# Kernel tuning notes

Hardware: AMD Instinct MI355X
Metric: run time of the kernel (lower is better)

## Reference

```python
import jax, jax.numpy as jnp
import numpy as np

B, T, D = 8, 16, 1024
N, K, H = 16, 8, 128   # q heads, kv heads, head dim
S = 8192               # cache size
CUR = 4096             # tokens already in cache
ROPE_THETA = 1000000
EPS = 1e-6
LARGE_NEGATIVE = jnp.finfo(jnp.bfloat16).min


def setup_inputs() -> dict:
    key = jax.random.key(0)
    ks = jax.random.split(key, 8)
    w = 0.02  # realistic weight scale
    return {
        "x": jax.random.normal(ks[0], (B, T, D), jnp.float32),
        "Wq": jax.random.normal(ks[1], (D, N, H), jnp.float32) * w,
        "Wk": jax.random.normal(ks[2], (D, K, H), jnp.float32) * w,
        "Wv": jax.random.normal(ks[3], (D, K, H), jnp.float32) * w,
        "Wo": jax.random.normal(ks[4], (N, H, D), jnp.float32) * w,
        "q_scale": jnp.ones((H,), jnp.float32),
        "k_scale": jnp.ones((H,), jnp.float32),
        "k_cache": jax.random.normal(ks[5], (B, S, K, H), jnp.float32),
        "v_cache": jax.random.normal(ks[6], (B, S, K, H), jnp.float32),
        "segment_ids": jnp.ones((B, T), jnp.int32),
        "start_ind": jnp.zeros((B,), jnp.int32),  # already resolved (= left_pads)
        "cur_ind": CUR,
    }


def _rmsnorm(x, scale, eps=EPS):
    xf = x.astype(jnp.float32)
    y = xf * jax.lax.rsqrt(jnp.mean(xf * xf, axis=-1, keepdims=True) + eps)
    return (y * scale).astype(x.dtype)


def _rope_sincos(positions, head_dim):
    frac = jnp.arange(0, head_dim, 2, dtype=jnp.float32) / head_dim
    inv_freq = 1.0 / (ROPE_THETA ** frac)
    ang = jnp.einsum("BT,k->BTk", positions.astype(jnp.float32), inv_freq,
                     precision=jax.lax.Precision.HIGHEST)
    return jnp.sin(ang), jnp.cos(ang)


def _apply_rope(x, sin, cos):
    x1, x2 = x[..., : x.shape[-1] // 2], x[..., x.shape[-1] // 2 :]
    sin, cos = sin[:, :, None, :], cos[:, :, None, :]
    return jnp.concatenate([x1 * cos - x2 * sin, x2 * cos + x1 * sin], axis=-1).astype(x.dtype)


def reference(x, Wq, Wk, Wv, Wo, q_scale, k_scale, k_cache, v_cache,
              segment_ids, start_ind, cur_ind):
    b, t, _ = x.shape
    n_rep = N // K
    scale = H ** -0.5

    # projections + per-head RMSNorm on q/k
    q = _rmsnorm(jnp.einsum("BTD,DNH->BTNH", x, Wq), q_scale)
    k = _rmsnorm(jnp.einsum("BSD,DKH->BSKH", x, Wk), k_scale)
    v = jnp.einsum("BSD,DKH->BSKH", x, Wv)

    # start index: resolved from left pads on first call
    left_pads = jnp.sum(jnp.cumsum(segment_ids != 0, axis=-1) == 0, -1).astype(jnp.int32)
    start = jnp.where(start_ind < 0, left_pads, start_ind)

    # positions from segment ids, offset by cache cursor
    rel = jax.vmap(lambda row: jnp.where(row != 0, jnp.arange(t) - jnp.argmax(row), 2 ** 30))(segment_ids)
    pos = rel + cur_ind
    sin, cos = _rope_sincos(pos, H)
    q = _apply_rope(q, sin, cos)
    k = _apply_rope(k, sin, cos)

    # KV cache append
    kc = jax.lax.dynamic_update_slice(k_cache, k, (0, cur_ind, 0, 0))
    vc = jax.lax.dynamic_update_slice(v_cache, v, (0, cur_ind, 0, 0))

    # GQA attention against full cache
    qg = q.reshape((b, t, K, n_rep, H))
    logits = jnp.einsum("BTKGH,BSKH->BTSKG", qg, kc) * scale

    q_pos = cur_ind + jnp.arange(t, dtype=jnp.int32)[None, :] - start[:, None]
    ts = jnp.arange(S, dtype=jnp.int32)
    kv_seg = (ts[None, :] >= start[:, None]) & (ts[None, :] < cur_ind + t)
    k_pos = ts[None, :] - start[:, None]
    causal = k_pos[:, None, :] <= q_pos[:, :, None]
    seg_mask = kv_seg[:, None, :] == segment_ids[:, :, None]
    mask = (causal & seg_mask)[:, :, :, None, None]

    logits = jnp.where(mask, logits, LARGE_NEGATIVE)
    w = jax.nn.softmax(logits.astype(jnp.float32), axis=2).astype(logits.dtype)
    o = jnp.einsum("BTSKG,BSKH->BTKGH", w, vc).reshape((b, t, N, H))
    return jnp.einsum("BTNH,NHD->BTD", o, Wo)
```

## Files before the change

kernel.cpp:

```cpp
#include <hip/hip_runtime.h>

#define BB 8
#define TT 16
#define DD 1024
#define NN 16
#define KHN 8
#define HH 128
#define SS 8192
#define NPART 16

typedef __attribute__((ext_vector_type(8))) short bf16x8;
typedef __attribute__((ext_vector_type(4))) float f32x4;

__device__ __forceinline__ unsigned short f2bf(float f) {
  unsigned u = __builtin_bit_cast(unsigned, f);
  u += 0x7FFFu + ((u >> 16) & 1u);
  return (unsigned short)(u >> 16);
}
__device__ __forceinline__ float bf2f(unsigned short h) {
  unsigned u = ((unsigned)h) << 16;
  return __builtin_bit_cast(float, u);
}
__device__ __forceinline__ f32x4 mfma16(bf16x8 a, bf16x8 b, f32x4 c) {
  return __builtin_amdgcn_mfma_f32_16x16x32_bf16(a, b, c, 0, 0, 0);
}
__device__ __forceinline__ unsigned cvt_pair(float a, float b) {
  unsigned r;
  asm("v_cvt_pk_bf16_f32 %0, %1, %2" : "=v"(r) : "v"(a), "v"(b));
  return r;
}
__device__ __forceinline__ void pack4(unsigned short* dst, float a, float b, float c, float d) {
  *(uint2*)dst = make_uint2(cvt_pair(a, b), cvt_pair(c, d));
}
__device__ __forceinline__ bf16x8 cvt8(const float4& lo, const float4& hi) {
  return __builtin_bit_cast(bf16x8,
      make_uint4(cvt_pair(lo.x, lo.y), cvt_pair(lo.z, lo.w),
                 cvt_pair(hi.x, hi.y), cvt_pair(hi.z, hi.w)));
}

__global__ __launch_bounds__(256) void k_wtrans(
    const float* __restrict__ Wq, const float* __restrict__ Wk,
    const float* __restrict__ Wv, const float* __restrict__ Wo,
    unsigned short* __restrict__ Wt1, unsigned short* __restrict__ Wt2) {
  __shared__ __align__(16) unsigned short Tl[64][66];
  const int tid = threadIdx.x;
  const int z = blockIdx.z;
  const float* src; int K, N; unsigned short* dst;
  if (z == 0)      { src = Wq; K = 1024; N = 2048; dst = Wt1; }
  else if (z == 1) { src = Wk; K = 1024; N = 1024; dst = Wt1 + (size_t)2048 * 1024; }
  else if (z == 2) { src = Wv; K = 1024; N = 1024; dst = Wt1 + (size_t)3072 * 1024; }
  else             { src = Wo; K = 2048; N = 1024; dst = Wt2; }
  const int n0 = blockIdx.x * 64, k0 = blockIdx.y * 64;
  if (n0 >= N || k0 >= K) return;
  {
    const int r = tid >> 4, c4 = (tid & 15) << 2;
#pragma unroll
    for (int p = 0; p < 4; ++p) {
      const int k = p * 16 + r;
      float4 f = *(const float4*)(src + (size_t)(k0 + k) * N + n0 + c4);
      pack4(&Tl[k][c4], f.x, f.y, f.z, f.w);
    }
  }
  __syncthreads();
  {
    const int c8 = tid & 7, nb = tid >> 3;
#pragma unroll
    for (int p = 0; p < 2; ++p) {
      const int n = p * 32 + nb;
      unsigned short tmp[8];
#pragma unroll
      for (int j = 0; j < 8; ++j) tmp[j] = Tl[c8 * 8 + j][n];
      unsigned short* dp = dst + (size_t)(n0 + n) * K + k0 + c8 * 8;
      *(uint4*)dp = *(const uint4*)&tmp[0];
    }
  }
}

__global__ __launch_bounds__(256) void k_qkv_gemm(
    const float* __restrict__ x, const unsigned short* __restrict__ Wt1,
    float* __restrict__ qkv) {
  const int tid = threadIdx.x, lane = tid & 63, wv = tid >> 6;
  const int cc = lane & 15, g = lane >> 4;
  const int m0 = blockIdx.x * 32, n0 = blockIdx.y * 128;
  const int rt = wv >> 1, cb0 = (wv & 1) * 64;
  const int m = m0 + rt * 16 + cc;
  f32x4 acc[4];
#pragma unroll
  for (int i = 0; i < 4; ++i) acc[i] = (f32x4)0.0f;

#pragma unroll 4
  for (int k0 = 0; k0 < 1024; k0 += 32) {
    float4 fa = *(const float4*)(x + (size_t)m * 1024 + k0 + g * 8);
    float4 fb = *(const float4*)(x + (size_t)m * 1024 + k0 + g * 8 + 4);
    bf16x8 af = cvt8(fa, fb);
#pragma unroll
    for (int ct = 0; ct < 4; ++ct) {
      const int n = n0 + cb0 + ct * 16 + cc;
      bf16x8 bf = *(const bf16x8*)(Wt1 + (size_t)n * 1024 + k0 + g * 8);
      acc[ct] = mfma16(af, bf, acc[ct]);
    }
  }
#pragma unroll
  for (int ct = 0; ct < 4; ++ct)
#pragma unroll
    for (int r = 0; r < 4; ++r) {
      int row = m0 + rt * 16 + g * 4 + r;
      int col = n0 + cb0 + ct * 16 + cc;
      qkv[(size_t)row * 4096 + col] = acc[ct][r];
    }
}

__global__ __launch_bounds__(128) void k_normrope(
    const float* __restrict__ qkv, const float* __restrict__ qs,
    const float* __restrict__ ks, const int* __restrict__ seg,
    const int* __restrict__ cur_p,
    unsigned short* __restrict__ qa, unsigned short* __restrict__ ka,
    unsigned short* __restrict__ va) {
  __shared__ float lv[128];
  __shared__ float red[2];
  const int row = blockIdx.x, b = row >> 4, t = row & 15;
  const int hid = blockIdx.y;
  const int h = threadIdx.x;
  float val;
  if (hid < 16)      val = qkv[row * 4096 + hid * 128 + h];
  else if (hid < 24) val = qkv[row * 4096 + 2048 + (hid - 16) * 128 + h];
  else               val = qkv[row * 4096 + 3072 + (hid - 24) * 128 + h];

  if (hid >= 24) {
    int kh = hid - 24;
    va[((b * KHN + kh) * TT + t) * 128 + h] = f2bf(val);
    return;
  }
  float ss = val * val;
#pragma unroll
  for (int m = 1; m < 64; m <<= 1) ss += __shfl_xor(ss, m, 64);
  int wid = threadIdx.x >> 6, lane = threadIdx.x & 63;
  if (lane == 0) red[wid] = ss;
  __syncthreads();
  float mean = (red[0] + red[1]) * (1.0f / 128.0f);
  float scl = (hid < 16) ? qs[h] : ks[h];
  float nrm = val * (1.0f / sqrtf(mean + 1e-6f)) * scl;
  lv[h] = nrm;
  __syncthreads();
  float prt = lv[h ^ 64];
  const int cur = cur_p[0];
  int first = TT;
#pragma unroll
  for (int i = TT - 1; i >= 0; --i)
    if (seg[b * TT + i] != 0) first = i;
  float posf;
  if (seg[b * TT + t] != 0) posf = (float)(t - first + cur);
  else                      posf = (float)(1073741824 + cur);
  int j = h & 63;
  float inv = powf(1.0e6f, -((float)j) * (1.0f / 64.0f));
  float ang = posf * inv;
  float sn = sinf(ang), cs = cosf(ang);
  float outv = (h < 64) ? (nrm * cs - prt * sn) : (nrm * cs + prt * sn);
  if (hid < 16) {
    int kh = hid >> 1, gq = hid & 1;
    qa[((b * KHN + kh) * 32 + gq * 16 + t) * 128 + h] =
        f2bf(outv * 0.08838834764831845f);
  } else {
    int kh = hid - 16;
    ka[((b * KHN + kh) * TT + t) * 128 + h] = f2bf(outv);
  }
}

__global__ __launch_bounds__(256, 2) void k_attn(
    const float* __restrict__ kcache, const float* __restrict__ vcache,
    const unsigned short* __restrict__ qa, const unsigned short* __restrict__ ka,
    const unsigned short* __restrict__ va, const int* __restrict__ seg,
    const int* __restrict__ sind, const int* __restrict__ cur_p,
    float* __restrict__ partO, float* __restrict__ partML) {
  __shared__ __align__(16) unsigned short Kl[4][32][132];
  __shared__ float mls[2][32][2];
  const int tid = threadIdx.x, wv = tid >> 6, lane = tid & 63;
  const int cc = lane & 15, g = lane >> 4;
  const int pair = blockIdx.x, b = pair >> 3, kh = pair & 7;
  const int qi = blockIdx.y;
  const int cur = cur_p[0];
  const int len = cur + TT;
  int start_b = sind[b];
  if (start_b < 0) {
    int first = TT;
#pragma unroll
    for (int i = TT - 1; i >= 0; --i)
      if (seg[b * TT + i] != 0) first = i;
    start_b = first;
  }
  const int NTt = (len + 31) >> 5;
  const int L = (NTt + NPART - 1) / NPART;
  const int tlo = qi * L;
  const int thi = (tlo + L < NTt) ? (tlo + L) : NTt;

  bf16x8 qf[2][4];
  {
    const unsigned short* qb = qa + ((size_t)pair * 32) * 128;
#pragma unroll
    for (int rb = 0; rb < 2; ++rb)
#pragma unroll
      for (int kk = 0; kk < 4; ++kk)
        qf[rb][kk] = *(const bf16x8*)(qb + (rb * 16 + cc) * 128 + kk * 32 + g * 8);
  }
  const float* kcb = kcache + (size_t)b * (SS * 1024) + kh * 128;
  const float* vcb = vcache + (size_t)b * (SS * 1024) + kh * 128;
  const unsigned short* knb = ka + (size_t)(b * KHN + kh) * (TT * 128);
  const unsigned short* vnb = va + (size_t)(b * KHN + kh) * (TT * 128);

  f32x4 acc[2][8];
  float mreg[2][4], lreg[2][4];
#pragma unroll
  for (int rb = 0; rb < 2; ++rb) {
#pragma unroll
    for (int hb = 0; hb < 8; ++hb) acc[rb][hb] = (f32x4)0.0f;
#pragma unroll
    for (int r = 0; r < 4; ++r) { mreg[rb][r] = -1e30f; lreg[rb][r] = 0.0f; }
  }

  for (int tile = tlo + wv; tile < thi; tile += 4) {
    const int ts0 = tile << 5;
    __builtin_amdgcn_wave_barrier();
    if (ts0 + 32 <= cur) {
#pragma unroll
      for (int i = 0; i < 16; ++i) {
        int ch = lane + (i << 6);
        int r = ch >> 5, c4 = (ch & 31) << 2;
        float4 f = *(const float4*)(kcb + (size_t)(ts0 + r) * 1024 + c4);
        pack4(&Kl[wv][r][c4], f.x, f.y, f.z, f.w);
      }
    } else {
#pragma unroll
      for (int i = 0; i < 16; ++i) {
        int ch = lane + (i << 6);
        int r = ch >> 5, c4 = (ch & 31) << 2;
        int ts = ts0 + r;
        if (ts < cur) {
          float4 f = *(const float4*)(kcb + (size_t)ts * 1024 + c4);
          pack4(&Kl[wv][r][c4], f.x, f.y, f.z, f.w);
        } else {
          int tr = ts - cur; if (tr > TT - 1) tr = TT - 1;
          ushort4 u = *(const ushort4*)(knb + tr * 128 + c4);
          *(ushort4*)&Kl[wv][r][c4] = u;
        }
      }
    }
    __builtin_amdgcn_wave_barrier();
    f32x4 s[2][2];
#pragma unroll
    for (int rb = 0; rb < 2; ++rb)
#pragma unroll
      for (int cb = 0; cb < 2; ++cb) s[rb][cb] = (f32x4)0.0f;
#pragma unroll
    for (int kk = 0; kk < 4; ++kk) {
#pragma unroll
      for (int cb = 0; cb < 2; ++cb) {
        const unsigned short* kp = &Kl[wv][cb * 16 + cc][kk * 32 + g * 8];
        uint2 lo = *(const uint2*)kp;
        uint2 hi = *(const uint2*)(kp + 4);
        bf16x8 kf = __builtin_bit_cast(bf16x8, make_uint4(lo.x, lo.y, hi.x, hi.y));
        s[0][cb] = mfma16(qf[0][kk], kf, s[0][cb]);
        s[1][cb] = mfma16(qf[1][kk], kf, s[1][cb]);
      }
    }
    bf16x8 vf[8];
    if (ts0 + 32 <= cur) {
#pragma unroll
      for (int hb = 0; hb < 8; ++hb) {
        const int hc = hb * 16 + cc;
        float v0 = vcb[(size_t)(ts0 + g * 8 + 0) * 1024 + hc];
        float v1 = vcb[(size_t)(ts0 + g * 8 + 1) * 1024 + hc];
        float v2 = vcb[(size_t)(ts0 + g * 8 + 2) * 1024 + hc];
        float v3 = vcb[(size_t)(ts0 + g * 8 + 3) * 1024 + hc];
        float v4 = vcb[(size_t)(ts0 + g * 8 + 4) * 1024 + hc];
        float v5 = vcb[(size_t)(ts0 + g * 8 + 5) * 1024 + hc];
        float v6 = vcb[(size_t)(ts0 + g * 8 + 6) * 1024 + hc];
        float v7 = vcb[(size_t)(ts0 + g * 8 + 7) * 1024 + hc];
        vf[hb] = __builtin_bit_cast(bf16x8,
            make_uint4(cvt_pair(v0, v1), cvt_pair(v2, v3),
                       cvt_pair(v4, v5), cvt_pair(v6, v7)));
      }
    } else {
#pragma unroll
      for (int hb = 0; hb < 8; ++hb) {
        const int hc = hb * 16 + cc;
        float vv[8];
#pragma unroll
        for (int j = 0; j < 8; ++j) {
          const int ts = ts0 + g * 8 + j;
          if (ts < cur) vv[j] = vcb[(size_t)ts * 1024 + hc];
          else { int tr = ts - cur; if (tr > TT - 1) tr = TT - 1; vv[j] = bf2f(vnb[tr * 128 + hc]); }
        }
        vf[hb] = __builtin_bit_cast(bf16x8,
            make_uint4(cvt_pair(vv[0], vv[1]), cvt_pair(vv[2], vv[3]),
                       cvt_pair(vv[4], vv[5]), cvt_pair(vv[6], vv[7])));
      }
    }
    float al[2][4];
#pragma unroll
    for (int rb = 0; rb < 2; ++rb) {
#pragma unroll
      for (int r = 0; r < 4; ++r) {
        const int tq = g * 4 + r;
#pragma unroll
        for (int cb = 0; cb < 2; ++cb) {
          int ts = ts0 + cb * 16 + cc;
          bool ok = (ts >= start_b) && (ts <= cur + tq);
          if (!ok) s[rb][cb][r] = -1e30f;
        }
        float tm = fmaxf(s[rb][0][r], s[rb][1][r]);
#pragma unroll
        for (int m = 1; m < 16; m <<= 1) tm = fmaxf(tm, __shfl_xor(tm, m, 64));
        float mn = fmaxf(mreg[rb][r], tm);
        float a = __expf(mreg[rb][r] - mn);
        float p0 = (s[rb][0][r] < -1e29f) ? 0.0f : __expf(s[rb][0][r] - mn);
        float p1 = (s[rb][1][r] < -1e29f) ? 0.0f : __expf(s[rb][1][r] - mn);
        s[rb][0][r] = p0; s[rb][1][r] = p1;
        float rs = p0 + p1;
#pragma unroll
        for (int m = 1; m < 16; m <<= 1) rs += __shfl_xor(rs, m, 64);
        lreg[rb][r] = lreg[rb][r] * a + rs;
        mreg[rb][r] = mn;
        al[rb][r] = a;
      }
    }
    __builtin_amdgcn_wave_barrier();
#pragma unroll
    for (int rb = 0; rb < 2; ++rb)
#pragma unroll
      for (int cb = 0; cb < 2; ++cb)
#pragma unroll
        for (int r = 0; r < 4; ++r)
          Kl[wv][rb * 16 + g * 4 + r][cb * 16 + cc] = f2bf(s[rb][cb][r]);
    __builtin_amdgcn_wave_barrier();
    bf16x8 pf[2];
#pragma unroll
    for (int rb = 0; rb < 2; ++rb) {
      const unsigned short* pp = &Kl[wv][rb * 16 + cc][g * 8];
      uint2 lo = *(const uint2*)pp;
      uint2 hi = *(const uint2*)(pp + 4);
      pf[rb] = __builtin_bit_cast(bf16x8, make_uint4(lo.x, lo.y, hi.x, hi.y));
    }
#pragma unroll
    for (int rb = 0; rb < 2; ++rb)
#pragma unroll
      for (int hb = 0; hb < 8; ++hb) {
        f32x4 t = acc[rb][hb];
#pragma unroll
        for (int r = 0; r < 4; ++r) t[r] *= al[rb][r];
        acc[rb][hb] = mfma16(pf[rb], vf[hb], t);
      }
  }

  float* Oscr = (float*)&Kl[0][0][0];
  auto dump = [&](int sid) {
#pragma unroll
    for (int rb = 0; rb < 2; ++rb)
#pragma unroll
      for (int hb = 0; hb < 8; ++hb)
#pragma unroll
        for (int r = 0; r < 4; ++r)
          Oscr[(sid * 32 + rb * 16 + g * 4 + r) * 128 + hb * 16 + cc] = acc[rb][hb][r];
    if (cc == 0) {
#pragma unroll
      for (int rb = 0; rb < 2; ++rb)
#pragma unroll
        for (int r = 0; r < 4; ++r) {
          mls[sid][rb * 16 + g * 4 + r][0] = mreg[rb][r];
          mls[sid][rb * 16 + g * 4 + r][1] = lreg[rb][r];
        }
    }
  };
  auto mergefrom = [&](int sid) {
    float a0s[2][4], a1s[2][4];
#pragma unroll
    for (int rb = 0; rb < 2; ++rb)
#pragma unroll
      for (int r = 0; r < 4; ++r) {
        int row = rb * 16 + g * 4 + r;
        float mp = mls[sid][row][0], lp = mls[sid][row][1];
        float M = fmaxf(mreg[rb][r], mp);
        float a0 = __expf(mreg[rb][r] - M), a1 = __expf(mp - M);
        lreg[rb][r] = lreg[rb][r] * a0 + lp * a1;
        mreg[rb][r] = M;
        a0s[rb][r] = a0; a1s[rb][r] = a1;
      }
#pragma unroll
    for (int rb = 0; rb < 2; ++rb)
#pragma unroll
      for (int hb = 0; hb < 8; ++hb)
#pragma unroll
        for (int r = 0; r < 4; ++r) {
          int row = rb * 16 + g * 4 + r;
          acc[rb][hb][r] = acc[rb][hb][r] * a0s[rb][r] +
                           Oscr[(sid * 32 + row) * 128 + hb * 16 + cc] * a1s[rb][r];
        }
  };
  __syncthreads();
  if (wv >= 2) dump(wv - 2);
  __syncthreads();
  if (wv < 2) mergefrom(wv);
  __syncthreads();
  if (wv == 1) dump(0);
  __syncthreads();
  if (wv == 0) {
    mergefrom(0);
    size_t pidx = (size_t)pair * NPART + qi;
#pragma unroll
    for (int rb = 0; rb < 2; ++rb)
#pragma unroll
      for (int hb = 0; hb < 8; ++hb)
#pragma unroll
        for (int r = 0; r < 4; ++r)
          partO[(pidx * 32 + rb * 16 + g * 4 + r) * 128 + hb * 16 + cc] = acc[rb][hb][r];
    if (cc == 0) {
#pragma unroll
      for (int rb = 0; rb < 2; ++rb)
#pragma unroll
        for (int r = 0; r < 4; ++r) {
          partML[pidx * 64 + (rb * 16 + g * 4 + r) * 2 + 0] = mreg[rb][r];
          partML[pidx * 64 + (rb * 16 + g * 4 + r) * 2 + 1] = lreg[rb][r];
        }
    }
  }
}

__global__ __launch_bounds__(256) void k_combine(
    const float* __restrict__ partO, const float* __restrict__ partML,
    unsigned short* __restrict__ obf) {
  __shared__ float sc[NPART][32];
  const int pair = blockIdx.x, b = pair >> 3, kh = pair & 7;
  const int isub = blockIdx.y;
  const int tid = threadIdx.x;
  if (tid < 32) {
    float mm[NPART], ll[NPART];
    float M = -3.0e38f;
#pragma unroll
    for (int p = 0; p < NPART; ++p) {
      mm[p] = partML[((size_t)pair * NPART + p) * 64 + tid * 2 + 0];
      ll[p] = partML[((size_t)pair * NPART + p) * 64 + tid * 2 + 1];
      M = fmaxf(M, mm[p]);
    }
    float denom = 0.0f;
#pragma unroll
    for (int p = 0; p < NPART; ++p) denom += __expf(mm[p] - M) * ll[p];
    float inv = (denom > 0.0f) ? 1.0f / denom : 0.0f;
#pragma unroll
    for (int p = 0; p < NPART; ++p) sc[p][tid] = __expf(mm[p] - M) * inv;
  }
  __syncthreads();
#pragma unroll
  for (int i = 0; i < 4; ++i) {
    int idx = tid + ((isub * 4 + i) << 8);
    int row = idx >> 7, hc = idx & 127;
    float o = 0.0f;
#pragma unroll
    for (int p = 0; p < NPART; ++p)
      o += partO[(((size_t)pair * NPART + p) * 32 + row) * 128 + hc] * sc[p][row];
    int gq = row >> 4, t = row & 15, n = kh * 2 + gq;
    obf[((b * TT + t) * NN + n) * 128 + hc] = f2bf(o);
  }
}

__global__ __launch_bounds__(256) void k_out_gemm(
    const unsigned short* __restrict__ obf, const unsigned short* __restrict__ Wt2,
    float* __restrict__ out) {
  const int tid = threadIdx.x, lane = tid & 63, wv = tid >> 6;
  const int cc = lane & 15, g = lane >> 4;
  const int m0 = blockIdx.x * 32, n0 = blockIdx.y * 64;
  const int rt = wv >> 1, cb0 = (wv & 1) * 32;
  const int m = m0 + rt * 16 + cc;
  f32x4 acc[2];
#pragma unroll
  for (int i = 0; i < 2; ++i) acc[i] = (f32x4)0.0f;

#pragma unroll 4
  for (int k0 = 0; k0 < 2048; k0 += 32) {
    bf16x8 af = *(const bf16x8*)(obf + (size_t)m * 2048 + k0 + g * 8);
#pragma unroll
    for (int ct = 0; ct < 2; ++ct) {
      const int d = n0 + cb0 + ct * 16 + cc;
      bf16x8 bf = *(const bf16x8*)(Wt2 + (size_t)d * 2048 + k0 + g * 8);
      acc[ct] = mfma16(af, bf, acc[ct]);
    }
  }
#pragma unroll
  for (int ct = 0; ct < 2; ++ct)
#pragma unroll
    for (int r = 0; r < 4; ++r)
      out[(size_t)(m0 + rt * 16 + g * 4 + r) * 1024 + n0 + cb0 + ct * 16 + cc] = acc[ct][r];
}

extern "C" void kernel_launch(void* const* d_in, const int* in_sizes, int n_in,
                              void* d_out, int out_size, void* d_ws, size_t ws_size,
                              hipStream_t stream) {
  (void)in_sizes; (void)n_in; (void)out_size; (void)ws_size;
  const float* x   = (const float*)d_in[0];
  const float* Wq  = (const float*)d_in[1];
  const float* Wk  = (const float*)d_in[2];
  const float* Wv  = (const float*)d_in[3];
  const float* Wo  = (const float*)d_in[4];
  const float* qs  = (const float*)d_in[5];
  const float* ks  = (const float*)d_in[6];
  const float* kc  = (const float*)d_in[7];
  const float* vc  = (const float*)d_in[8];
  const int* seg   = (const int*)d_in[9];
  const int* sind  = (const int*)d_in[10];
  const int* curp  = (const int*)d_in[11];
  float* out = (float*)d_out;

  char* ws = (char*)d_ws;
  float*          qkv    = (float*)(ws + 0);
  unsigned short* qa     = (unsigned short*)(ws + 2097152);
  unsigned short* ka     = (unsigned short*)(ws + 2621440);
  unsigned short* va     = (unsigned short*)(ws + 2883584);
  float*          partO  = (float*)(ws + 3145728);
  float*          partML = (float*)(ws + 19922944);
  unsigned short* obf    = (unsigned short*)(ws + 20185088);
  unsigned short* Wt1    = (unsigned short*)(ws + 20709376);
  unsigned short* Wt2    = (unsigned short*)(ws + 29097984);

  k_wtrans<<<dim3(32, 32, 4), 256, 0, stream>>>(Wq, Wk, Wv, Wo, Wt1, Wt2);
  k_qkv_gemm<<<dim3(4, 32), 256, 0, stream>>>(x, Wt1, qkv);
  k_normrope<<<dim3(128, 32), 128, 0, stream>>>(qkv, qs, ks, seg, curp, qa, ka, va);
  k_attn<<<dim3(64, NPART), 256, 0, stream>>>(kc, vc, qa, ka, va, seg, sind, curp, partO, partML);
  k_combine<<<dim3(64, 4), 256, 0, stream>>>(partO, partML, obf);
  k_out_gemm<<<dim3(4, 16), 256, 0, stream>>>(obf, Wt2, out);
}
```

Baseline: 151.4 us.

## Prefetch next K tile into registers and halve attention split partitions

Adds software pipelining in the attention kernel: the K tile for the next iteration is loaded into registers during the current iteration and written to LDS after the P fragment is read. A separate LDS buffer for P replaces the reuse of the K buffer so the prefetched K write does not conflict. It also halves the number of KV partitions per (batch, kv-head), giving each block more tiles to amortize setup and shrinking the partial buffers, with workspace offsets adjusted. In exchange it holds 16 float4 registers per thread, which may cut occupancy, and halves the grid size.

```diff
diff --git a/kernel.cpp b/kernel.cpp
--- a/kernel.cpp
+++ b/kernel.cpp
@@ -7,7 +7,7 @@
 #define KHN 8
 #define HH 128
 #define SS 8192
-#define NPART 16
+#define NPART 8
 
 typedef __attribute__((ext_vector_type(8))) short bf16x8;
 typedef __attribute__((ext_vector_type(4))) float f32x4;
@@ -166,6 +166,43 @@
   }
 }
 
+#define KLOAD(TILE)                                                          \
+  do {                                                                       \
+    const int ts0_ = (TILE) << 5;                                            \
+    _Pragma("unroll")                                                        \
+    for (int i_ = 0; i_ < 16; ++i_) {                                        \
+      const int ch_ = lane + (i_ << 6);                                      \
+      const int r_ = ch_ >> 5, c4_ = (ch_ & 31) << 2;                        \
+      const int ts_ = ts0_ + r_;                                             \
+      if (ts_ < cur) {                                                       \
+        kreg[i_] = *(const float4*)(kcb + (size_t)ts_ * 1024 + c4_);         \
+      } else {                                                               \
+        int tr_ = ts_ - cur; if (tr_ > TT - 1) tr_ = TT - 1;                 \
+        uint2 w_ = *(const uint2*)(knb + tr_ * 128 + c4_);                   \
+        kreg[i_].x = __builtin_bit_cast(float, w_.x);                        \
+        kreg[i_].y = __builtin_bit_cast(float, w_.y);                        \
+      }                                                                      \
+    }                                                                        \
+  } while (0)
+
+#define KWRITE(TILE)                                                         \
+  do {                                                                       \
+    const int ts0_ = (TILE) << 5;                                            \
+    _Pragma("unroll")                                                        \
+    for (int i_ = 0; i_ < 16; ++i_) {                                        \
+      const int ch_ = lane + (i_ << 6);                                      \
+      const int r_ = ch_ >> 5, c4_ = (ch_ & 31) << 2;                        \
+      const int ts_ = ts0_ + r_;                                             \
+      if (ts_ < cur) {                                                       \
+        pack4(&Kl[wv][r_][c4_], kreg[i_].x, kreg[i_].y, kreg[i_].z, kreg[i_].w); \
+      } else {                                                               \
+        *(uint2*)&Kl[wv][r_][c4_] =                                          \
+            make_uint2(__builtin_bit_cast(unsigned, kreg[i_].x),             \
+                       __builtin_bit_cast(unsigned, kreg[i_].y));            \
+      }                                                                      \
+    }                                                                        \
+  } while (0)
+
 __global__ __launch_bounds__(256, 2) void k_attn(
     const float* __restrict__ kcache, const float* __restrict__ vcache,
     const unsigned short* __restrict__ qa, const unsigned short* __restrict__ ka,
@@ -173,6 +210,7 @@
     const int* __restrict__ sind, const int* __restrict__ cur_p,
     float* __restrict__ partO, float* __restrict__ partML) {
   __shared__ __align__(16) unsigned short Kl[4][32][132];
+  __shared__ __align__(16) unsigned short Pl[4][32][40];
   __shared__ float mls[2][32][2];
   const int tid = threadIdx.x, wv = tid >> 6, lane = tid & 63;
   const int cc = lane & 15, g = lane >> 4;
@@ -217,33 +255,13 @@
     for (int r = 0; r < 4; ++r) { mreg[rb][r] = -1e30f; lreg[rb][r] = 0.0f; }
   }
 
-  for (int tile = tlo + wv; tile < thi; tile += 4) {
+  float4 kreg[16];
+  const int t0 = tlo + wv;
+  if (t0 < thi) { KLOAD(t0); KWRITE(t0); }
+
+  for (int tile = t0; tile < thi; tile += 4) {
     const int ts0 = tile << 5;
-    __builtin_amdgcn_wave_barrier();
-    if (ts0 + 32 <= cur) {
-#pragma unroll
-      for (int i = 0; i < 16; ++i) {
-        int ch = lane + (i << 6);
-        int r = ch >> 5, c4 = (ch & 31) << 2;
-        float4 f = *(const float4*)(kcb + (size_t)(ts0 + r) * 1024 + c4);
-        pack4(&Kl[wv][r][c4], f.x, f.y, f.z, f.w);
-      }
-    } else {
-#pragma unroll
-      for (int i = 0; i < 16; ++i) {
-        int ch = lane + (i << 6);
-        int r = ch >> 5, c4 = (ch & 31) << 2;
-        int ts = ts0 + r;
-        if (ts < cur) {
-          float4 f = *(const float4*)(kcb + (size_t)ts * 1024 + c4);
-          pack4(&Kl[wv][r][c4], f.x, f.y, f.z, f.w);
-        } else {
-          int tr = ts - cur; if (tr > TT - 1) tr = TT - 1;
-          ushort4 u = *(const ushort4*)(knb + tr * 128 + c4);
-          *(ushort4*)&Kl[wv][r][c4] = u;
-        }
-      }
-    }
+    const bool pfetch = (tile + 4 < thi);
     __builtin_amdgcn_wave_barrier();
     f32x4 s[2][2];
 #pragma unroll
@@ -295,6 +313,10 @@
                        cvt_pair(vv[4], vv[5]), cvt_pair(vv[6], vv[7])));
       }
     }
+    if (pfetch) {
+      KLOAD(tile + 4);
+      __builtin_amdgcn_sched_barrier(0);
+    }
     float al[2][4];
 #pragma unroll
     for (int rb = 0; rb < 2; ++rb) {
@@ -323,23 +345,19 @@
         al[rb][r] = a;
       }
     }
-    __builtin_amdgcn_wave_barrier();
 #pragma unroll
     for (int rb = 0; rb < 2; ++rb)
 #pragma unroll
       for (int cb = 0; cb < 2; ++cb)
 #pragma unroll
         for (int r = 0; r < 4; ++r)
-          Kl[wv][rb * 16 + g * 4 + r][cb * 16 + cc] = f2bf(s[rb][cb][r]);
+          Pl[wv][rb * 16 + g * 4 + r][cb * 16 + cc] = f2bf(s[rb][cb][r]);
     __builtin_amdgcn_wave_barrier();
     bf16x8 pf[2];
 #pragma unroll
-    for (int rb = 0; rb < 2; ++rb) {
-      const unsigned short* pp = &Kl[wv][rb * 16 + cc][g * 8];
-      uint2 lo = *(const uint2*)pp;
-      uint2 hi = *(const uint2*)(pp + 4);
-      pf[rb] = __builtin_bit_cast(bf16x8, make_uint4(lo.x, lo.y, hi.x, hi.y));
-    }
+    for (int rb = 0; rb < 2; ++rb)
+      pf[rb] = *(const bf16x8*)&Pl[wv][rb * 16 + cc][g * 8];
+    if (pfetch) KWRITE(tile + 4);
 #pragma unroll
     for (int rb = 0; rb < 2; ++rb)
 #pragma unroll
@@ -514,10 +532,10 @@
   unsigned short* ka     = (unsigned short*)(ws + 2621440);
   unsigned short* va     = (unsigned short*)(ws + 2883584);
   float*          partO  = (float*)(ws + 3145728);
-  float*          partML = (float*)(ws + 19922944);
-  unsigned short* obf    = (unsigned short*)(ws + 20185088);
-  unsigned short* Wt1    = (unsigned short*)(ws + 20709376);
-  unsigned short* Wt2    = (unsigned short*)(ws + 29097984);
+  float*          partML = (float*)(ws + 11534336);
+  unsigned short* obf    = (unsigned short*)(ws + 11665408);
+  unsigned short* Wt1    = (unsigned short*)(ws + 12189696);
+  unsigned short* Wt2    = (unsigned short*)(ws + 20578304);
 
   k_wtrans<<<dim3(32, 32, 4), 256, 0, stream>>>(Wq, Wk, Wv, Wo, Wt1, Wt2);
   k_qkv_gemm<<<dim3(4, 32), 256, 0, stream>>>(x, Wt1, qkv);
```

After: 246.6 us. 62.9% more time.

## Halve attention partitions, add unmasked softmax fast path, separate P buffer

Applied to the files above, without the earlier changes.

Cuts the split-KV partition count from 16 to 8, shrinking the partial-output workspace and the combine work but halving the attention grid to 512 blocks. Adds a fast path that skips mask checks and sentinel comparisons for tiles that are fully interior and past start. Moves the probability tile to a dedicated 16-byte-aligned shared buffer, so it loads with a single vector read and the wave barrier before the write can be dropped. The smaller grid may reduce parallelism for the memory-bound cache streaming.

```diff
diff --git a/kernel.cpp b/kernel.cpp
--- a/kernel.cpp
+++ b/kernel.cpp
@@ -7,7 +7,7 @@
 #define KHN 8
 #define HH 128
 #define SS 8192
-#define NPART 16
+#define NPART 8
 
 typedef __attribute__((ext_vector_type(8))) short bf16x8;
 typedef __attribute__((ext_vector_type(4))) float f32x4;
@@ -173,6 +173,7 @@
     const int* __restrict__ sind, const int* __restrict__ cur_p,
     float* __restrict__ partO, float* __restrict__ partML) {
   __shared__ __align__(16) unsigned short Kl[4][32][132];
+  __shared__ __align__(16) unsigned short Pl[4][32][40];
   __shared__ float mls[2][32][2];
   const int tid = threadIdx.x, wv = tid >> 6, lane = tid & 63;
   const int cc = lane & 15, g = lane >> 4;
@@ -219,8 +220,10 @@
 
   for (int tile = tlo + wv; tile < thi; tile += 4) {
     const int ts0 = tile << 5;
+    const bool interior = (ts0 + 32 <= cur);
+    const bool allvis = interior && (ts0 >= start_b);
     __builtin_amdgcn_wave_barrier();
-    if (ts0 + 32 <= cur) {
+    if (interior) {
 #pragma unroll
       for (int i = 0; i < 16; ++i) {
         int ch = lane + (i << 6);
@@ -263,7 +266,7 @@
       }
     }
     bf16x8 vf[8];
-    if (ts0 + 32 <= cur) {
+    if (interior) {
 #pragma unroll
       for (int hb = 0; hb < 8; ++hb) {
         const int hc = hb * 16 + cc;
@@ -296,50 +299,68 @@
       }
     }
     float al[2][4];
-#pragma unroll
-    for (int rb = 0; rb < 2; ++rb) {
-#pragma unroll
-      for (int r = 0; r < 4; ++r) {
-        const int tq = g * 4 + r;
-#pragma unroll
-        for (int cb = 0; cb < 2; ++cb) {
-          int ts = ts0 + cb * 16 + cc;
-          bool ok = (ts >= start_b) && (ts <= cur + tq);
-          if (!ok) s[rb][cb][r] = -1e30f;
-        }
-        float tm = fmaxf(s[rb][0][r], s[rb][1][r]);
-#pragma unroll
-        for (int m = 1; m < 16; m <<= 1) tm = fmaxf(tm, __shfl_xor(tm, m, 64));
-        float mn = fmaxf(mreg[rb][r], tm);
-        float a = __expf(mreg[rb][r] - mn);
-        float p0 = (s[rb][0][r] < -1e29f) ? 0.0f : __expf(s[rb][0][r] - mn);
-        float p1 = (s[rb][1][r] < -1e29f) ? 0.0f : __expf(s[rb][1][r] - mn);
-        s[rb][0][r] = p0; s[rb][1][r] = p1;
-        float rs = p0 + p1;
-#pragma unroll
-        for (int m = 1; m < 16; m <<= 1) rs += __shfl_xor(rs, m, 64);
-        lreg[rb][r] = lreg[rb][r] * a + rs;
-        mreg[rb][r] = mn;
-        al[rb][r] = a;
-      }
-    }
-    __builtin_amdgcn_wave_barrier();
+    if (allvis) {
+#pragma unroll
+      for (int rb = 0; rb < 2; ++rb) {
+#pragma unroll
+        for (int r = 0; r < 4; ++r) {
+          float tm = fmaxf(s[rb][0][r], s[rb][1][r]);
+#pragma unroll
+          for (int m = 1; m < 16; m <<= 1) tm = fmaxf(tm, __shfl_xor(tm, m, 64));
+          float mn = fmaxf(mreg[rb][r], tm);
+          float a = __expf(mreg[rb][r] - mn);
+          float p0 = __expf(s[rb][0][r] - mn);
+          float p1 = __expf(s[rb][1][r] - mn);
+          s[rb][0][r] = p0; s[rb][1][r] = p1;
+          float rs = p0 + p1;
+#pragma unroll
+          for (int m = 1; m < 16; m <<= 1) rs += __shfl_xor(rs, m, 64);
+          lreg[rb][r] = lreg[rb][r] * a + rs;
+          mreg[rb][r] = mn;
+          al[rb][r] = a;
+        }
+      }
+    } else {
+#pragma unroll
+      for (int rb = 0; rb < 2; ++rb) {
+#pragma unroll
+        for (int r = 0; r < 4; ++r) {
+          const int tq = g * 4 + r;
+#pragma unroll
+          for (int cb = 0; cb < 2; ++cb) {
+            int ts = ts0 + cb * 16 + cc;
+            bool ok = (ts >= start_b) && (ts <= cur + tq);
+            if (!ok) s[rb][cb][r] = -1e30f;
+          }
+          float tm = fmaxf(s[rb][0][r], s[rb][1][r]);
+#pragma unroll
+          for (int m = 1; m < 16; m <<= 1) tm = fmaxf(tm, __shfl_xor(tm, m, 64));
+          float mn = fmaxf(mreg[rb][r], tm);
+          float a = __expf(mreg[rb][r] - mn);
+          float p0 = (s[rb][0][r] < -1e29f) ? 0.0f : __expf(s[rb][0][r] - mn);
+          float p1 = (s[rb][1][r] < -1e29f) ? 0.0f : __expf(s[rb][1][r] - mn);
+          s[rb][0][r] = p0; s[rb][1][r] = p1;
+          float rs = p0 + p1;
+#pragma unroll
+          for (int m = 1; m < 16; m <<= 1) rs += __shfl_xor(rs, m, 64);
+          lreg[rb][r] = lreg[rb][r] * a + rs;
+          mreg[rb][r] = mn;
+          al[rb][r] = a;
+        }
+      }
+    }
 #pragma unroll
     for (int rb = 0; rb < 2; ++rb)
 #pragma unroll
       for (int cb = 0; cb < 2; ++cb)
 #pragma unroll
         for (int r = 0; r < 4; ++r)
-          Kl[wv][rb * 16 + g * 4 + r][cb * 16 + cc] = f2bf(s[rb][cb][r]);
+          Pl[wv][rb * 16 + g * 4 + r][cb * 16 + cc] = f2bf(s[rb][cb][r]);
     __builtin_amdgcn_wave_barrier();
     bf16x8 pf[2];
 #pragma unroll
-    for (int rb = 0; rb < 2; ++rb) {
-      const unsigned short* pp = &Kl[wv][rb * 16 + cc][g * 8];
-      uint2 lo = *(const uint2*)pp;
-      uint2 hi = *(const uint2*)(pp + 4);
-      pf[rb] = __builtin_bit_cast(bf16x8, make_uint4(lo.x, lo.y, hi.x, hi.y));
-    }
+    for (int rb = 0; rb < 2; ++rb)
+      pf[rb] = *(const bf16x8*)&Pl[wv][rb * 16 + cc][g * 8];
 #pragma unroll
     for (int rb = 0; rb < 2; ++rb)
 #pragma unroll
@@ -514,10 +535,10 @@
   unsigned short* ka     = (unsigned short*)(ws + 2621440);
   unsigned short* va     = (unsigned short*)(ws + 2883584);
   float*          partO  = (float*)(ws + 3145728);
-  float*          partML = (float*)(ws + 19922944);
-  unsigned short* obf    = (unsigned short*)(ws + 20185088);
-  unsigned short* Wt1    = (unsigned short*)(ws + 20709376);
-  unsigned short* Wt2    = (unsigned short*)(ws + 29097984);
+  float*          partML = (float*)(ws + 11534336);
+  unsigned short* obf    = (unsigned short*)(ws + 11665408);
+  unsigned short* Wt1    = (unsigned short*)(ws + 12189696);
+  unsigned short* Wt2    = (unsigned short*)(ws + 20578304);
 
   k_wtrans<<<dim3(32, 32, 4), 256, 0, stream>>>(Wq, Wk, Wv, Wo, Wt1, Wt2);
   k_qkv_gemm<<<dim3(4, 32), 256, 0, stream>>>(x, Wt1, qkv);
```

Measured after the change: 158.7 us. 4.8% more time.
